# Kernel tuning notes

Measured on AMD Instinct MI355X. Metric: run time of the kernel, lower is better.

The kernel has to match this reference:

```python
import jax, jax.numpy as jnp
import numpy as np

HEADS = 32
DK = 32            # att_size = hidden // heads
CUT = 15.5         # tot_dis[cur_layer=0] + 0.5
NEG = -1e8
LN_EPS = 1e-5


def layernorm(x, g, b):
    m = jnp.mean(x, axis=-1, keepdims=True)
    v = jnp.mean((x - m) ** 2, axis=-1, keepdims=True)
    return (x - m) / jnp.sqrt(v + LN_EPS) * g + b


def setup_inputs() -> dict:
    key = jax.random.key(0)
    ks = jax.random.split(key, 12)
    B, S, H, F = 8, 513, 1024, 4096
    N = S - 1
    def nrm(k, shape, scale=0.02):
        return jax.random.normal(k, shape, jnp.float32) * scale
    x = jax.random.normal(ks[0], (B, S, H), jnp.float32)
    attn_bias = jax.random.normal(ks[1], (B, HEADS, S, S), jnp.float32)
    rel_pos = jax.random.randint(ks[2], (B, N, N), 0, 16, jnp.int32)
    rel_emb = nrm(ks[3], (512, HEADS)).at[0].set(0.0)  # padding_idx=0
    Wq = nrm(ks[4], (H, H)); bq = jnp.zeros((H,), jnp.float32)
    Wk = nrm(ks[5], (H, H)); bk = jnp.zeros((H,), jnp.float32)
    Wv = nrm(ks[6], (H, H)); bv = jnp.zeros((H,), jnp.float32)
    Wo = nrm(ks[7], (H, H)); bo = jnp.zeros((H,), jnp.float32)
    W1 = nrm(ks[8], (H, F)); b1 = jnp.zeros((F,), jnp.float32)
    W2 = nrm(ks[9], (F, H)); b2 = jnp.zeros((H,), jnp.float32)
    ln1_g = jnp.ones((H,), jnp.float32); ln1_b = jnp.zeros((H,), jnp.float32)
    ln2_g = jnp.ones((H,), jnp.float32); ln2_b = jnp.zeros((H,), jnp.float32)
    return dict(x=x, attn_bias=attn_bias, rel_emb=rel_emb,
                Wq=Wq, bq=bq, Wk=Wk, bk=bk, Wv=Wv, bv=bv, Wo=Wo, bo=bo,
                W1=W1, b1=b1, W2=W2, b2=b2,
                ln1_g=ln1_g, ln1_b=ln1_b, ln2_g=ln2_g, ln2_b=ln2_b,
                rel_pos=rel_pos)


def reference(x, attn_bias, rel_emb, Wq, bq, Wk, bk, Wv, bv, Wo, bo,
              W1, b1, W2, b2, ln1_g, ln1_b, ln2_g, ln2_b, rel_pos):
    B, S, H = x.shape
    # rel-pos bias: embed [B,N,N] -> [B,N,N,heads] -> [B,heads,N,N]
    rpb = jnp.transpose(rel_emb[rel_pos], (0, 3, 1, 2))
    inner = attn_bias[:, :, 1:, 1:] + rpb
    # per-head mask flag: keep if within cutoff distance OR already -inf-masked
    flags = (rel_pos[:, None, :, :] <= CUT) | (inner < NEG)
    ab = attn_bias.at[:, :, 1:, 1:].set(inner * flags)
    # attention
    y = layernorm(x, ln1_g, ln1_b)
    scale = DK ** -0.5
    q = (y @ Wq + bq).reshape(B, S, HEADS, DK) * scale
    k = (y @ Wk + bk).reshape(B, S, HEADS, DK)
    v = (y @ Wv + bv).reshape(B, S, HEADS, DK)
    scores = jnp.einsum('bqhd,bkhd->bhqk', q, k) + ab
    attn = jax.nn.softmax(scores, axis=-1)
    o = jnp.einsum('bhqk,bkhd->bqhd', attn, v).reshape(B, S, H)
    x = x + (o @ Wo + bo)
    # FFN
    y = layernorm(x, ln2_g, ln2_b)
    y = jax.nn.gelu(y @ W1 + b1, approximate=False) @ W2 + b2
    return x + y
```

## Files before the change

### kernel.cpp

```cpp
#include <hip/hip_runtime.h>
#include <hip/hip_bf16.h>
#include <math.h>

typedef __attribute__((ext_vector_type(8))) short short8;
typedef __attribute__((ext_vector_type(4))) float f32x4;
typedef unsigned short u16;
typedef unsigned int u32;

#define SQ 513
#define MPAD 4224
#define MV 4104
#define NHEADS 32
#define DKH 32
#define SVP 576

static __device__ inline u16 f2bf(float f) {
  u32 u = __builtin_bit_cast(u32, f);
  u = (u + 0x7fffu + ((u >> 16) & 1u)) >> 16;
  return (u16)u;
}

static __device__ inline void gld16(const void* g, void* l) {
  __builtin_amdgcn_global_load_lds((__attribute__((address_space(1))) void*)g,
                                   (__attribute__((address_space(3))) void*)l,
                                   16, 0, 0);
}

static __device__ inline float gelu_f(float x) {
  return 0.5f * x * (1.f + erff(x * 0.70710678118654752f));
}

__global__ __launch_bounds__(256) void transpose_cast_k(const float* __restrict__ in,
    u16* __restrict__ out, int K, int N, float scale)
{
  __shared__ float t[32][33];
  int n0 = blockIdx.x * 32, k0 = blockIdx.y * 32;
  int tx = threadIdx.x & 31, ty = threadIdx.x >> 5;
#pragma unroll
  for (int i = 0; i < 32; i += 8)
    t[ty + i][tx] = in[(size_t)(k0 + ty + i) * N + n0 + tx];
  __syncthreads();
#pragma unroll
  for (int i = 0; i < 32; i += 8)
    out[(size_t)(n0 + ty + i) * K + k0 + tx] = f2bf(t[tx][ty + i] * scale);
}

__global__ __launch_bounds__(256) void vtrans_k(const u16* __restrict__ qkv,
    u16* __restrict__ vT)
{
  __shared__ u16 t[32][33];
  int st = blockIdx.x * 32, h = blockIdx.y, b = blockIdx.z;
  int tx = threadIdx.x & 31, ty = threadIdx.x >> 5;
#pragma unroll
  for (int i = 0; i < 32; i += 8) {
    int s = st + ty + i;
    int sc = s > 512 ? 512 : s;
    t[ty + i][tx] = qkv[(size_t)(b * SQ + sc) * 3072 + 2048 + h * DKH + tx];
  }
  __syncthreads();
#pragma unroll
  for (int i = 0; i < 32; i += 8) {
    int d = ty + i;
    vT[(((size_t)b * NHEADS + h) * DKH + d) * SVP + st + tx] = t[tx][d];
  }
}

__global__ __launch_bounds__(256) void prep_bias_k(const float* __restrict__ bq,
    const float* __restrict__ bk, const float* __restrict__ bv,
    float* __restrict__ out, float scale)
{
  int i = blockIdx.x * 256 + threadIdx.x;
  float v = (i < 1024) ? bq[i] * scale : ((i < 2048) ? bk[i - 1024] : bv[i - 2048]);
  out[i] = v;
}

__global__ __launch_bounds__(256) void ln_k(const float* __restrict__ in,
    const float* __restrict__ g, const float* __restrict__ b,
    u16* __restrict__ out)
{
  int row = blockIdx.x;
  float4 v = ((const float4*)(in + (size_t)row * 1024))[threadIdx.x];
  float s = v.x + v.y + v.z + v.w;
  float s2 = v.x * v.x + v.y * v.y + v.z * v.z + v.w * v.w;
#pragma unroll
  for (int d = 32; d; d >>= 1) { s += __shfl_xor(s, d, 64); s2 += __shfl_xor(s2, d, 64); }
  __shared__ float ps[4], ps2[4];
  int w = threadIdx.x >> 6;
  if ((threadIdx.x & 63) == 0) { ps[w] = s; ps2[w] = s2; }
  __syncthreads();
  s = ps[0] + ps[1] + ps[2] + ps[3];
  s2 = ps2[0] + ps2[1] + ps2[2] + ps2[3];
  float mean = s * (1.f / 1024.f);
  float var = s2 * (1.f / 1024.f) - mean * mean;
  float inv = rsqrtf(var + 1e-5f);
  float4 gv = ((const float4*)g)[threadIdx.x];
  float4 bv = ((const float4*)b)[threadIdx.x];
  ushort4 o;
  o.x = f2bf((v.x - mean) * inv * gv.x + bv.x);
  o.y = f2bf((v.y - mean) * inv * gv.y + bv.y);
  o.z = f2bf((v.z - mean) * inv * gv.z + bv.z);
  o.w = f2bf((v.w - mean) * inv * gv.w + bv.w);
  ((ushort4*)(out + (size_t)row * 1024))[threadIdx.x] = o;
}

template <int EPI>
__global__ __launch_bounds__(256) void gemm_bt(const u16* __restrict__ A,
    const u16* __restrict__ Bw, const float* __restrict__ bias,
    const float* __restrict__ resid, void* __restrict__ outp,
    int N, int K, int nbx)
{
  __shared__ alignas(16) u16 sA[128 * 64];
  __shared__ alignas(16) u16 sB[128 * 64];
  int tid = threadIdx.x;
  int l = tid & 63, lg = l >> 4, li = l & 15;
  int mb = blockIdx.x / nbx, nb = blockIdx.x % nbx;
  int m0 = mb * 128, n0 = nb * 128;
  int wv = tid >> 6;
  int wr = wv >> 1, wc = wv & 1;
  f32x4 acc[4][4] = {};
  int r_ = tid >> 3, c_ = (tid & 7) * 8;
  const u16* Ag = A + (size_t)(m0 + r_) * K + c_;
  const u16* Bg = Bw + (size_t)(n0 + r_) * K + c_;
  u16* sAb = sA + (tid & 192) * 8;
  u16* sBb = sB + (tid & 192) * 8;

  for (int k0 = 0; k0 < K; k0 += 64) {
    __syncthreads();
#pragma unroll
    for (int i = 0; i < 4; ++i) {
      gld16(Ag + (size_t)(i * 32) * K + k0, sAb + i * 2048);
      gld16(Bg + (size_t)(i * 32) * K + k0, sBb + i * 2048);
    }
    __syncthreads();
#pragma unroll
    for (int ks = 0; ks < 2; ++ks) {
      short8 af[4], bfr[4];
#pragma unroll
      for (int i = 0; i < 4; ++i)
        af[i] = *(const short8*)&sA[(64 * wr + 16 * i + li) * 64 + ks * 32 + lg * 8];
#pragma unroll
      for (int j = 0; j < 4; ++j)
        bfr[j] = *(const short8*)&sB[(64 * wc + 16 * j + li) * 64 + ks * 32 + lg * 8];
#pragma unroll
      for (int i = 0; i < 4; ++i)
#pragma unroll
        for (int j = 0; j < 4; ++j)
          acc[i][j] = __builtin_amdgcn_mfma_f32_16x16x32_bf16(af[i], bfr[j], acc[i][j], 0, 0, 0);
    }
  }

#pragma unroll
  for (int i = 0; i < 4; ++i) {
    int rb = m0 + 64 * wr + 16 * i + 4 * lg;
#pragma unroll
    for (int j = 0; j < 4; ++j) {
      int col = n0 + 64 * wc + 16 * j + li;
      float bia = bias[col];
#pragma unroll
      for (int r = 0; r < 4; ++r) {
        int row = rb + r;
        float v = acc[i][j][r] + bia;
        if (EPI == 0) {
          ((u16*)outp)[(size_t)row * N + col] = f2bf(v);
        } else if (EPI == 1) {
          if (row < MV) {
            v += resid[(size_t)row * N + col];
            ((float*)outp)[(size_t)row * N + col] = v;
          }
        } else if (EPI == 2) {
          ((u16*)outp)[(size_t)row * N + col] = f2bf(gelu_f(v));
        } else {
          if (row < MV) ((float*)outp)[(size_t)row * N + col] += v;
        }
      }
    }
  }
}

__global__ __launch_bounds__(256) void attn_fused(const u16* __restrict__ qkv,
    const u16* __restrict__ vT, const float* __restrict__ attn_bias,
    const int* __restrict__ rel_pos, const float* __restrict__ rel_emb,
    u16* __restrict__ o)
{
  __shared__ alignas(16) u16 p_lds[4][16][72];
  int bid = blockIdx.x;
  int qt = bid % 9, h = (bid / 9) % NHEADS, b = bid / (9 * NHEADS);
  int tid = threadIdx.x, wv = tid >> 6, l = tid & 63, lg = l >> 4, li = l & 15;
  int q0 = qt * 64;
  int sqb = q0 + 16 * wv + 4 * lg;

  short8 qfrag = *(const short8*)(qkv + (size_t)(b * SQ + q0 + 16 * wv + li) * 3072 + h * DKH + lg * 8);

  float tv = rel_emb[(size_t)li * NHEADS + h];

  const float* bias_row[4];
  const int* rp_row[4];
#pragma unroll
  for (int r = 0; r < 4; ++r) {
    int sq = sqb + r;
    int sqc = sq > 512 ? 512 : sq;
    bias_row[r] = attn_bias + (((size_t)b * NHEADS + h) * SQ + sqc) * SQ;
    int sqm = sq - 1; sqm = sqm < 0 ? 0 : (sqm > 511 ? 511 : sqm);
    rp_row[r] = rel_pos + ((size_t)b * 512 + sqm) * 512;
  }

  const u16* kfb = qkv + (size_t)(b * SQ) * 3072 + 1024 + h * DKH + lg * 8;
  const u16* vtb = vT + (((size_t)b * NHEADS + h) * DKH) * SVP + lg * 8;

  short8 kf[4], vb[4];
  float pb[4][4];
  int pr[4][4];

#pragma unroll
  for (int f = 0; f < 4; ++f)
    kf[f] = *(const short8*)(kfb + (size_t)(16 * f + li) * 3072);
#pragma unroll
  for (int u = 0; u < 4; ++u) {
    int df = u >> 1, kk = u & 1;
    vb[u] = *(const short8*)(vtb + (size_t)(16 * df + li) * SVP + kk * 32);
  }
#pragma unroll
  for (int f = 0; f < 4; ++f) {
    int sk = 16 * f + li;
    int skm = sk - 1; skm = skm < 0 ? 0 : skm;
#pragma unroll
    for (int r = 0; r < 4; ++r) {
      pb[f][r] = bias_row[r][sk];
      pr[f][r] = rp_row[r][skm];
    }
  }

  f32x4 o_acc[2] = {};
  float m_run[4], l_run[4];
#pragma unroll
  for (int r = 0; r < 4; ++r) { m_run[r] = -1e30f; l_run[r] = 0.f; }

  for (int kt = 0; kt < 9; ++kt) {
    f32x4 sc[4];
#pragma unroll
    for (int f = 0; f < 4; ++f) {
      f32x4 z = {};
      sc[f] = __builtin_amdgcn_mfma_f32_16x16x32_bf16(qfrag, kf[f], z, 0, 0, 0);
    }
    if (kt < 8) {
      const u16* kfn = kfb + (size_t)((kt + 1) * 64) * 3072;
#pragma unroll
      for (int f = 0; f < 4; ++f)
        kf[f] = *(const short8*)(kfn + (size_t)(16 * f + li) * 3072);
    }

#pragma unroll
    for (int f = 0; f < 4; ++f) {
      int sk = kt * 64 + 16 * f + li;
#pragma unroll
      for (int r = 0; r < 4; ++r) {
        int sq = sqb + r;
        float base = pb[f][r];
        int rp = pr[f][r];
        float re = __shfl(tv, rp, 64);
        float inner = base + re;
        float ab = (rp <= 15 || inner < -1e8f) ? inner : 0.f;
        if (sq == 0 || sk == 0) ab = base;
        if (sq > 512 || sk > 512) ab = -1e30f;
        sc[f][r] += ab;
      }
    }
    if (kt < 8) {
#pragma unroll
      for (int f = 0; f < 4; ++f) {
        int sk = (kt + 1) * 64 + 16 * f + li;
        int skc = sk > 512 ? 512 : sk;
        int skm = sk - 1; skm = skm > 511 ? 511 : skm;
#pragma unroll
        for (int r = 0; r < 4; ++r) {
          pb[f][r] = bias_row[r][skc];
          pr[f][r] = rp_row[r][skm];
        }
      }
    }

    float alpha[4];
#pragma unroll
    for (int r = 0; r < 4; ++r) {
      float mx = fmaxf(fmaxf(sc[0][r], sc[1][r]), fmaxf(sc[2][r], sc[3][r]));
#pragma unroll
      for (int d = 1; d < 16; d <<= 1) mx = fmaxf(mx, __shfl_xor(mx, d, 16));
      float mn = fmaxf(m_run[r], mx);
      alpha[r] = __expf(m_run[r] - mn);
      m_run[r] = mn;
      l_run[r] *= alpha[r];
    }
#pragma unroll
    for (int f = 0; f < 4; ++f)
#pragma unroll
      for (int r = 0; r < 4; ++r) {
        float p = __expf(sc[f][r] - m_run[r]);
        l_run[r] += p;
        p_lds[wv][4 * lg + r][16 * f + li] = f2bf(p);
      }
#pragma unroll
    for (int df = 0; df < 2; ++df)
#pragma unroll
      for (int r = 0; r < 4; ++r) o_acc[df][r] *= alpha[r];

#pragma unroll
    for (int kk = 0; kk < 2; ++kk) {
      short8 pa = *(const short8*)&p_lds[wv][li][kk * 32 + lg * 8];
#pragma unroll
      for (int df = 0; df < 2; ++df)
        o_acc[df] = __builtin_amdgcn_mfma_f32_16x16x32_bf16(pa, vb[df * 2 + kk], o_acc[df], 0, 0, 0);
    }
    if (kt < 8) {
      const u16* vtn = vtb + (kt + 1) * 64;
#pragma unroll
      for (int u = 0; u < 4; ++u) {
        int df = u >> 1, kk = u & 1;
        vb[u] = *(const short8*)(vtn + (size_t)(16 * df + li) * SVP + kk * 32);
      }
    }
  }

#pragma unroll
  for (int r = 0; r < 4; ++r) {
    float s = l_run[r];
#pragma unroll
    for (int d = 1; d < 16; d <<= 1) s += __shfl_xor(s, d, 16);
    l_run[r] = s;
  }
#pragma unroll
  for (int df = 0; df < 2; ++df)
#pragma unroll
    for (int r = 0; r < 4; ++r) {
      int s_q = sqb + r;
      if (s_q <= 512)
        o[(size_t)(b * SQ + s_q) * 1024 + h * DKH + 16 * df + li] = f2bf(o_acc[df][r] / l_run[r]);
    }
}

extern "C" void kernel_launch(void* const* d_in, const int* in_sizes, int n_in,
                              void* d_out, int out_size, void* d_ws, size_t ws_size,
                              hipStream_t stream) {
  const float* x        = (const float*)d_in[0];
  const float* attn_bias= (const float*)d_in[1];
  const float* rel_emb  = (const float*)d_in[2];
  const float* Wq = (const float*)d_in[3];
  const float* bq = (const float*)d_in[4];
  const float* Wk = (const float*)d_in[5];
  const float* bk = (const float*)d_in[6];
  const float* Wv = (const float*)d_in[7];
  const float* bv = (const float*)d_in[8];
  const float* Wo = (const float*)d_in[9];
  const float* bo = (const float*)d_in[10];
  const float* W1 = (const float*)d_in[11];
  const float* b1 = (const float*)d_in[12];
  const float* W2 = (const float*)d_in[13];
  const float* b2 = (const float*)d_in[14];
  const float* ln1g = (const float*)d_in[15];
  const float* ln1b = (const float*)d_in[16];
  const float* ln2g = (const float*)d_in[17];
  const float* ln2b = (const float*)d_in[18];
  const int*   rel_pos = (const int*)d_in[19];
  float* out = (float*)d_out;

  char* ws = (char*)d_ws;
  size_t off = 0;
  auto alloc = [&](size_t bytes) { char* p = ws + off; off += (bytes + 255) & ~(size_t)255; return p; };
  u16* w_qkvT = (u16*)alloc((size_t)3072 * 1024 * 2);
  u16* w_oT   = (u16*)alloc((size_t)1024 * 1024 * 2);
  u16* w_1T   = (u16*)alloc((size_t)4096 * 1024 * 2);
  u16* w_2T   = (u16*)alloc((size_t)1024 * 4096 * 2);
  float* bias_qkv = (float*)alloc(3072 * 4);
  u16* ybuf = (u16*)alloc((size_t)MPAD * 1024 * 2);
  u16* obuf = (u16*)alloc((size_t)MPAD * 1024 * 2);
  u16* vTb  = (u16*)alloc((size_t)8 * NHEADS * DKH * SVP * 2);
  u16* big  = (u16*)alloc((size_t)MPAD * 4096 * 2);

  const float scale = 0.17677669529663689f;
  dim3 blk(256);

  transpose_cast_k<<<dim3(32, 32), blk, 0, stream>>>(Wq, w_qkvT, 1024, 1024, scale);
  transpose_cast_k<<<dim3(32, 32), blk, 0, stream>>>(Wk, w_qkvT + (size_t)1024 * 1024, 1024, 1024, 1.f);
  transpose_cast_k<<<dim3(32, 32), blk, 0, stream>>>(Wv, w_qkvT + (size_t)2048 * 1024, 1024, 1024, 1.f);
  transpose_cast_k<<<dim3(32, 32), blk, 0, stream>>>(Wo, w_oT, 1024, 1024, 1.f);
  transpose_cast_k<<<dim3(128, 32), blk, 0, stream>>>(W1, w_1T, 1024, 4096, 1.f);
  transpose_cast_k<<<dim3(32, 128), blk, 0, stream>>>(W2, w_2T, 4096, 1024, 1.f);
  prep_bias_k<<<12, blk, 0, stream>>>(bq, bk, bv, bias_qkv, scale);

  ln_k<<<MV, blk, 0, stream>>>(x, ln1g, ln1b, ybuf);
  gemm_bt<0><<<33 * 24, blk, 0, stream>>>(ybuf, w_qkvT, bias_qkv, nullptr, big, 3072, 1024, 24);
  vtrans_k<<<dim3(18, NHEADS, 8), blk, 0, stream>>>(big, vTb);
  attn_fused<<<8 * NHEADS * 9, blk, 0, stream>>>(big, vTb, attn_bias, rel_pos, rel_emb, obuf);
  gemm_bt<1><<<33 * 8, blk, 0, stream>>>(obuf, w_oT, bo, x, out, 1024, 1024, 8);
  ln_k<<<MV, blk, 0, stream>>>(out, ln2g, ln2b, ybuf);
  gemm_bt<2><<<33 * 32, blk, 0, stream>>>(ybuf, w_1T, b1, nullptr, big, 4096, 1024, 32);
  gemm_bt<3><<<33 * 8, blk, 0, stream>>>(big, w_2T, b2, nullptr, out, 1024, 4096, 8);
}
```

Before: 549.0 us.

## Stage K and V tiles through double-buffered swizzled LDS in attention kernel

```diff
diff --git a/kernel.cpp b/kernel.cpp
--- a/kernel.cpp
+++ b/kernel.cpp
@@ -182,6 +182,8 @@
     const int* __restrict__ rel_pos, const float* __restrict__ rel_emb,
     u16* __restrict__ o)
 {
+  __shared__ alignas(16) u16 k_lds[2][64 * 32];
+  __shared__ alignas(16) u16 v_lds[2][32 * 64];
   __shared__ alignas(16) u16 p_lds[4][16][72];
   int bid = blockIdx.x;
   int qt = bid % 9, h = (bid / 9) % NHEADS, b = bid / (9 * NHEADS);
@@ -204,21 +206,28 @@
     rp_row[r] = rel_pos + ((size_t)b * 512 + sqm) * 512;
   }
 
-  const u16* kfb = qkv + (size_t)(b * SQ) * 3072 + 1024 + h * DKH + lg * 8;
-  const u16* vtb = vT + (((size_t)b * NHEADS + h) * DKH) * SVP + lg * 8;
-
-  short8 kf[4], vb[4];
+  int krow = tid >> 2;
+  int kchunk = (tid & 3) ^ ((tid >> 3) & 3);
+  const u16* ksrc = qkv + (size_t)(b * SQ) * 3072 + 1024 + h * DKH + kchunk * 8;
+  int vrow = tid >> 3;
+  int vchunk = (tid & 7) ^ (vrow & 7);
+  const u16* vsrc = vT + (((size_t)b * NHEADS + h) * DKH + vrow) * SVP + vchunk * 8;
+
+  int koff[4], voff[4];
+#pragma unroll
+  for (int f = 0; f < 4; ++f)
+    koff[f] = (16 * f + li) * 32 + ((lg ^ ((li >> 1) & 3)) * 8);
+#pragma unroll
+  for (int u = 0; u < 4; ++u) {
+    int df = u >> 1, kk = u & 1;
+    voff[u] = (16 * df + li) * 64 + (((kk * 4 + lg) ^ (li & 7)) * 8);
+  }
+
   float pb[4][4];
   int pr[4][4];
 
-#pragma unroll
-  for (int f = 0; f < 4; ++f)
-    kf[f] = *(const short8*)(kfb + (size_t)(16 * f + li) * 3072);
-#pragma unroll
-  for (int u = 0; u < 4; ++u) {
-    int df = u >> 1, kk = u & 1;
-    vb[u] = *(const short8*)(vtb + (size_t)(16 * df + li) * SVP + kk * 32);
-  }
+  gld16(ksrc + (size_t)krow * 3072, (u16*)k_lds[0] + tid * 8);
+  gld16(vsrc, (u16*)v_lds[0] + tid * 8);
 #pragma unroll
   for (int f = 0; f < 4; ++f) {
     int sk = 16 * f + li;
@@ -236,17 +245,22 @@
   for (int r = 0; r < 4; ++r) { m_run[r] = -1e30f; l_run[r] = 0.f; }
 
   for (int kt = 0; kt < 9; ++kt) {
+    int cur = kt & 1;
+    __syncthreads();
+    if (kt < 8) {
+      int s = (kt + 1) * 64 + krow; if (s > 512) s = 512;
+      gld16(ksrc + (size_t)s * 3072, (u16*)k_lds[cur ^ 1] + tid * 8);
+      gld16(vsrc + (size_t)(kt + 1) * 64, (u16*)v_lds[cur ^ 1] + tid * 8);
+    }
+    const u16* kb = k_lds[cur];
+    const u16* vbf = v_lds[cur];
+
     f32x4 sc[4];
 #pragma unroll
     for (int f = 0; f < 4; ++f) {
+      short8 kf = *(const short8*)&kb[koff[f]];
       f32x4 z = {};
-      sc[f] = __builtin_amdgcn_mfma_f32_16x16x32_bf16(qfrag, kf[f], z, 0, 0, 0);
-    }
-    if (kt < 8) {
-      const u16* kfn = kfb + (size_t)((kt + 1) * 64) * 3072;
-#pragma unroll
-      for (int f = 0; f < 4; ++f)
-        kf[f] = *(const short8*)(kfn + (size_t)(16 * f + li) * 3072);
+      sc[f] = __builtin_amdgcn_mfma_f32_16x16x32_bf16(qfrag, kf, z, 0, 0, 0);
     }
 
 #pragma unroll
@@ -307,15 +321,9 @@
     for (int kk = 0; kk < 2; ++kk) {
       short8 pa = *(const short8*)&p_lds[wv][li][kk * 32 + lg * 8];
 #pragma unroll
-      for (int df = 0; df < 2; ++df)
-        o_acc[df] = __builtin_amdgcn_mfma_f32_16x16x32_bf16(pa, vb[df * 2 + kk], o_acc[df], 0, 0, 0);
-    }
-    if (kt < 8) {
-      const u16* vtn = vtb + (kt + 1) * 64;
-#pragma unroll
-      for (int u = 0; u < 4; ++u) {
-        int df = u >> 1, kk = u & 1;
-        vb[u] = *(const short8*)(vtn + (size_t)(16 * df + li) * SVP + kk * 32);
+      for (int df = 0; df < 2; ++df) {
+        short8 vb = *(const short8*)&vbf[voff[df * 2 + kk]];
+        o_acc[df] = __builtin_amdgcn_mfma_f32_16x16x32_bf16(pa, vb, o_acc[df], 0, 0, 0);
       }
     }
   }
```

Result: faster. 499.4 us (-9.0%).
